# Optimization experiments

Measured on AMD Instinct MI355X. Metric: run time of the kernel, lower is better.

The kernel has to match this reference:

```python
import jax, jax.numpy as jnp
import numpy as np

HEAD = 8
C = 32  # dhead
SCALE = 0.17677669529663687  # 1/sqrt(32)


def setup_inputs() -> dict:
    key = jax.random.key(0)
    k1, k2, k3, k4 = jax.random.split(key, 4)
    N, S, R, M = 1, 256, 384, 256
    msa_repr = jax.random.normal(k1, (N, S, R, M), dtype=jnp.float32)
    # 0.02 init scale keeps softmax logits / sigmoid pre-activations in a sane range
    gate_proj = jax.random.normal(k2, (M, M), dtype=jnp.float32) * 0.02
    qkv_proj = jax.random.normal(k3, (M, 3 * M), dtype=jnp.float32) * 0.02
    out_proj = jax.random.normal(k4, (M, M), dtype=jnp.float32) * 0.02
    return {"msa_repr": msa_repr, "gate_proj": gate_proj, "qkv_proj": qkv_proj, "out_proj": out_proj}


def reference(msa_repr, gate_proj, qkv_proj, out_proj):
    # col_attn: permute [N,S,R,M] -> [N,R,S,M]; attention runs over the residue axis S
    x = jnp.transpose(msa_repr, (0, 2, 1, 3))  # [N,R,S,M]
    N, R, S, M = x.shape
    gate = jax.nn.sigmoid(x @ gate_proj).reshape(N, R, S, HEAD, C)
    q, k, v = jnp.split(x @ qkv_proj, 3, axis=-1)  # each [N,R,S,M]
    q = q.reshape(N, R, S, HEAD, C)
    k = k.reshape(N, R, S, HEAD, C)
    v = v.reshape(N, R, S, HEAD, C)
    sim = jnp.einsum('nrihc,nrjhc->nrhij', q, k) * jnp.float32(SCALE)  # [N,R,H,S,S]
    attn = jax.nn.softmax(sim, axis=-1)
    out = jnp.einsum('nrhij,nrjhc->nrihc', attn, v) * gate  # [N,R,S,H,C]
    out = out.reshape(N, R, S, HEAD * C) @ out_proj  # [N,R,S,M]
    return jnp.transpose(out, (0, 2, 1, 3))  # back to [N,S,R,M]
```

## Files before the change

### kernel.cpp

```cpp
#include <hip/hip_runtime.h>
#include <hip/hip_bf16.h>

#define R_DIM 384
#define S_DIM 256
#define M_DIM 256

typedef __attribute__((ext_vector_type(4))) float  f32x4;
typedef __attribute__((ext_vector_type(4))) float  fvec4;
typedef __attribute__((ext_vector_type(8))) short  short8;
typedef __attribute__((ext_vector_type(4))) short  short4v;

__device__ __forceinline__ short f2bf(float f) {
    __hip_bfloat16 h = __float2bfloat16(f);
    return __builtin_bit_cast(short, h);
}
__device__ __forceinline__ float bf2f(short s) {
    return __bfloat162float(__builtin_bit_cast(__hip_bfloat16, s));
}

__device__ __forceinline__ void gload_lds16(const void* gsrc, void* ldst) {
    __builtin_amdgcn_global_load_lds(
        (const __attribute__((address_space(1))) unsigned int*)gsrc,
        (__attribute__((address_space(3))) unsigned int*)ldst, 16, 0, 0);
}

#define QSCALE (0.17677669529663687f * 1.4426950408889634f)

__global__ __launch_bounds__(256) void k_prep(
    const float* __restrict__ gp, const float* __restrict__ qkvp,
    const float* __restrict__ op, short* __restrict__ Wt1,
    short* __restrict__ Wot)
{
    __shared__ float tile[64][65];
    const int tx = threadIdx.x & 63, ty = threadIdx.x >> 6;
    const int k0 = blockIdx.x * 64;
    const int j0 = blockIdx.y * 64;
    const float* src; int ld, cb;
    if (j0 < 256)       { src = gp;   ld = 256; cb = j0; }
    else if (j0 < 1024) { src = qkvp; ld = 768; cb = j0 - 256; }
    else                { src = op;   ld = 256; cb = j0 - 1024; }
    for (int q = 0; q < 16; ++q) {
        const int kk = q * 4 + ty;
        tile[kk][tx] = src[(k0 + kk) * ld + cb + tx];
    }
    __syncthreads();
    for (int q = 0; q < 16; ++q) {
        const int jj = q * 4 + ty;
        const int jglob = j0 + jj;
        const float scl = (jglob >= 256 && jglob < 512) ? QSCALE : 1.0f;
        const float val = tile[tx][jj] * scl;
        if (jglob < 1024) Wt1[jglob * 256 + k0 + tx] = f2bf(val);
        else              Wot[(jglob - 1024) * 256 + k0 + tx] = f2bf(val);
    }
}

__global__ __launch_bounds__(256, 3) void k_qkvgate(
    const float* __restrict__ msa, const short* __restrict__ Wt1,
    short* __restrict__ gate, short* __restrict__ qb,
    short* __restrict__ kb, short* __restrict__ vb)
{
    __shared__ __align__(16) char Al[64 * 512];
    __shared__ __align__(16) short Bl[2][128 * 32];
    const int tid = threadIdx.x;
    const int l = tid & 63, w = tid >> 6;
    const int wr = w >> 1, wc = w & 1;
    const int rowBase = blockIdx.x * 64;

    {
        const int arow0 = tid >> 6;
        const int col4  = (tid & 63) * 4;
        const int slot  = (tid & 63) >> 1;
        const int sub   = (tid & 63) & 1;
        for (int ii = 0; ii < 16; ++ii) {
            const int a_r = ii * 4 + arow0;
            const int i = rowBase + a_r;
            const int rr = i >> 8, ss = i & 255;
            fvec4 vv = *(const fvec4*)(msa + ((ss * R_DIM + rr) << 8) + col4);
            short4v b4;
            b4.x = f2bf(vv.x); b4.y = f2bf(vv.y);
            b4.z = f2bf(vv.z); b4.w = f2bf(vv.w);
            *(short4v*)(Al + a_r * 512 + ((slot ^ (a_r & 7)) << 4) + sub * 8) = b4;
        }
    }

    auto stageB = [&](int tt, short* buf) {
        const int cb = (tt >> 3) * 128, k0 = (tt & 7) * 32;
        #pragma unroll
        for (int r = 0; r < 2; ++r) {
            const int L = r * 256 + w * 64 + l;
            const int row = L >> 2, psl = L & 3;
            const int gsl = psl ^ ((row >> 1) & 3);
            gload_lds16(Wt1 + (cb + row) * 256 + k0 + gsl * 8,
                        buf + (r * 256 + w * 64) * 8);
        }
    };

    stageB(0, (short*)Bl[0]);
    __syncthreads();

    short8 af[8][2];
    #pragma unroll
    for (int kc = 0; kc < 8; ++kc) {
        const int aslot = kc * 4 + (l >> 4);
        #pragma unroll
        for (int it = 0; it < 2; ++it) {
            const int row = wr * 32 + it * 16 + (l & 15);
            af[kc][it] = *(const short8*)(Al + row * 512 + ((aslot ^ (row & 7)) << 4));
        }
    }

    short* AlT = (short*)Al;
    const int rr_blk = rowBase >> 8;
    const int ssBase = rowBase & 255;

    f32x4 acc[2][4] = {};
    for (int ct = 0; ct < 8; ++ct) {
        #pragma unroll
        for (int kc = 0; kc < 8; ++kc) {
            const int t = ct * 8 + kc;
            if (t + 1 < 64) stageB(t + 1, (short*)Bl[(kc + 1) & 1]);

            const short* Bb = (const short*)Bl[kc & 1];
            short8 bfr[4];
            #pragma unroll
            for (int jt = 0; jt < 4; ++jt) {
                const int row = wc * 64 + jt * 16 + (l & 15);
                const int psl = (l >> 4) ^ ((row >> 1) & 3);
                bfr[jt] = *(const short8*)(Bb + row * 32 + psl * 8);
            }
            #pragma unroll
            for (int it = 0; it < 2; ++it)
                #pragma unroll
                for (int jt = 0; jt < 4; ++jt)
                    acc[it][jt] = __builtin_amdgcn_mfma_f32_16x16x32_bf16(
                        af[kc][it], bfr[jt], acc[it][jt], 0, 0, 0);

            __syncthreads();
        }
        const int colBase = ct * 128;
        const int sel = ct >> 1;
        if (sel < 3) {
            short* dst = (sel == 0) ? gate : (sel == 1) ? qb : kb;
            #pragma unroll
            for (int it = 0; it < 2; ++it) {
                const int base_i = rowBase + wr * 32 + it * 16 + ((l >> 4) << 2);
                #pragma unroll
                for (int reg = 0; reg < 4; ++reg) {
                    const int i = base_i + reg;
                    const int rr = i >> 8, ss = i & 255;
                    #pragma unroll
                    for (int jt = 0; jt < 4; ++jt) {
                        const int jg = colBase + wc * 64 + jt * 16 + (l & 15);
                        const int jj = jg & 255;
                        const int h = jj >> 5, c = jj & 31;
                        float vv = acc[it][jt][reg];
                        if (sel == 0) vv = 1.0f / (1.0f + __builtin_amdgcn_exp2f(-vv * 1.4426950408889634f));
                        dst[(((rr << 3) + h) * 256 + ss) * 32 + c] = f2bf(vv);
                    }
                }
            }
        } else {
            const int jjBase = (colBase & 255);
            #pragma unroll
            for (int it = 0; it < 2; ++it) {
                const int ssL0 = wr * 32 + it * 16 + ((l >> 4) << 2);
                #pragma unroll
                for (int reg = 0; reg < 4; ++reg) {
                    #pragma unroll
                    for (int jt = 0; jt < 4; ++jt) {
                        const int jjL = wc * 64 + jt * 16 + (l & 15);
                        AlT[jjL * 72 + ssL0 + reg] = f2bf(acc[it][jt][reg]);
                    }
                }
            }
            __syncthreads();
            #pragma unroll
            for (int q = 0; q < 4; ++q) {
                const int cid = q * 256 + tid;
                const int jjL = cid >> 3, sc = cid & 7;
                short8 vv8 = *(const short8*)(&AlT[jjL * 72 + sc * 8]);
                const int jj = jjBase + jjL;
                const int h = jj >> 5, c = jj & 31;
                const int pp = (rr_blk << 3) + h;
                *(short8*)(vb + (pp << 13) + (c << 8) + ssBase + sc * 8) = vv8;
            }
        }
        #pragma unroll
        for (int it = 0; it < 2; ++it)
            #pragma unroll
            for (int jt = 0; jt < 4; ++jt)
                acc[it][jt] = (f32x4){0.f, 0.f, 0.f, 0.f};
    }
}

__global__ __launch_bounds__(256) void k_attn(
    short* qo, const short* __restrict__ kb, const short* __restrict__ vb,
    const short* __restrict__ gate)
{
    __shared__ __align__(16) short Pl[4 * 32 * 68];
    const int tid = threadIdx.x;
    const int l = tid & 63, w = tid >> 6;
    const int p = blockIdx.x;
    short* qg = qo + p * 8192;
    const short* kg = kb + p * 8192;
    const short* vg = vb + p * 8192;
    const short* gg = gate + p * 8192;
    const int c0 = (l >> 4) * 8;

    short8 qf[4];
    #pragma unroll
    for (int it = 0; it < 4; ++it) {
        const int s = w * 64 + it * 16 + (l & 15);
        qf[it] = *(const short8*)(qg + s * 32 + c0);
    }

    f32x4 oacc[4][2] = {};
    f32x4 ssum[4] = {};
    short8 bones;
    #pragma unroll
    for (int e = 0; e < 8; ++e) bones[e] = (short)0x3F80;
    short* Pw = &Pl[w * (32 * 68)];

    for (int ch = 0; ch < 4; ++ch) {
        const int j0 = ch * 64;
        f32x4 sacc[4][4] = {};
        short8 kf[4];
        #pragma unroll
        for (int jt = 0; jt < 4; ++jt) {
            const int row = j0 + jt * 16 + (l & 15);
            kf[jt] = *(const short8*)(kg + row * 32 + c0);
        }
        #pragma unroll
        for (int it = 0; it < 4; ++it)
            #pragma unroll
            for (int jt = 0; jt < 4; ++jt)
                sacc[it][jt] = __builtin_amdgcn_mfma_f32_16x16x32_bf16(
                    qf[it], kf[jt], sacc[it][jt], 0, 0, 0);

        short8 vfa[2][2];
        #pragma unroll
        for (int kk = 0; kk < 2; ++kk)
            #pragma unroll
            for (int cti = 0; cti < 2; ++cti)
                vfa[kk][cti] = *(const short8*)(
                    vg + (cti * 16 + (l & 15)) * 256 + j0 + kk * 32 + (l >> 4) * 8);

        #pragma unroll
        for (int ih = 0; ih < 2; ++ih) {
            #pragma unroll
            for (int itl = 0; itl < 2; ++itl) {
                const int it = ih * 2 + itl;
                #pragma unroll
                for (int reg = 0; reg < 4; ++reg) {
                    const int rowl = itl * 16 + ((l >> 4) << 2) + reg;
                    #pragma unroll
                    for (int jt = 0; jt < 4; ++jt)
                        Pw[rowl * 68 + jt * 16 + (l & 15)] =
                            f2bf(__builtin_amdgcn_exp2f(sacc[it][jt][reg]));
                }
            }
            #pragma unroll
            for (int kk = 0; kk < 2; ++kk) {
                const int koff = kk * 32 + (l >> 4) * 8;
                short8 pf[2];
                #pragma unroll
                for (int itl = 0; itl < 2; ++itl)
                    pf[itl] = *(const short8*)(&Pw[(itl * 16 + (l & 15)) * 68 + koff]);
                #pragma unroll
                for (int itl = 0; itl < 2; ++itl) {
                    const int it = ih * 2 + itl;
                    #pragma unroll
                    for (int cti = 0; cti < 2; ++cti)
                        oacc[it][cti] = __builtin_amdgcn_mfma_f32_16x16x32_bf16(
                            pf[itl], vfa[kk][cti], oacc[it][cti], 0, 0, 0);
                    ssum[it] = __builtin_amdgcn_mfma_f32_16x16x32_bf16(
                        pf[itl], bones, ssum[it], 0, 0, 0);
                }
            }
        }
    }
    #pragma unroll
    for (int it = 0; it < 4; ++it) {
        #pragma unroll
        for (int reg = 0; reg < 4; ++reg) {
            const float inv = 1.0f / ssum[it][reg];
            const int s = w * 64 + it * 16 + ((l >> 4) << 2) + reg;
            #pragma unroll
            for (int cti = 0; cti < 2; ++cti) {
                const int c = cti * 16 + (l & 15);
                const float gv = bf2f(gg[s * 32 + c]);
                qg[s * 32 + c] = f2bf(oacc[it][cti][reg] * inv * gv);
            }
        }
    }
}

__global__ __launch_bounds__(256) void k_out(
    const short* __restrict__ ao, const short* __restrict__ Wot,
    float* __restrict__ out)
{
    __shared__ __align__(16) char Al[128 * 128];
    __shared__ __align__(16) char Bl[128 * 128];
    const int tid = threadIdx.x;
    const int l = tid & 63, w = tid >> 6;
    const int wr = w >> 1, wc = w & 1;
    const int rowBase = blockIdx.y * 128;
    const int colBase = blockIdx.x * 128;
    f32x4 acc[4][4] = {};
    for (int kidx = 0; kidx < 4; ++kidx) {
        const int k0 = kidx * 64;
        {
            const int slot = tid & 7;
            const int rb = tid >> 3;
            const int kin = k0 + slot * 8;
            const int h = kin >> 5, c0 = kin & 31;
            #pragma unroll
            for (int ii = 0; ii < 4; ++ii) {
                const int a_r = ii * 32 + rb;
                const int i = rowBase + a_r;
                const int rr = i >> 8, ss = i & 255;
                short8 av = *(const short8*)(ao + (((rr << 3) + h) * 256 + ss) * 32 + c0);
                *(short8*)(Al + a_r * 128 + ((slot ^ (a_r & 7)) << 4)) = av;
            }
            #pragma unroll
            for (int jj = 0; jj < 4; ++jj) {
                const int j_r = jj * 32 + rb;
                short8 wv = *(const short8*)(Wot + (colBase + j_r) * 256 + k0 + slot * 8);
                *(short8*)(Bl + j_r * 128 + ((slot ^ (j_r & 7)) << 4)) = wv;
            }
        }
        __syncthreads();
        #pragma unroll
        for (int kh = 0; kh < 2; ++kh) {
            short8 af[4], bfr[4];
            const int sl = kh * 4 + (l >> 4);
            #pragma unroll
            for (int it = 0; it < 4; ++it) {
                const int row = wr * 64 + it * 16 + (l & 15);
                af[it] = *(const short8*)(Al + row * 128 + ((sl ^ (row & 7)) << 4));
            }
            #pragma unroll
            for (int jt = 0; jt < 4; ++jt) {
                const int row = wc * 64 + jt * 16 + (l & 15);
                bfr[jt] = *(const short8*)(Bl + row * 128 + ((sl ^ (row & 7)) << 4));
            }
            #pragma unroll
            for (int it = 0; it < 4; ++it)
                #pragma unroll
                for (int jt = 0; jt < 4; ++jt)
                    acc[it][jt] = __builtin_amdgcn_mfma_f32_16x16x32_bf16(
                        af[it], bfr[jt], acc[it][jt], 0, 0, 0);
        }
        __syncthreads();
    }
    #pragma unroll
    for (int it = 0; it < 4; ++it) {
        const int base_i = rowBase + wr * 64 + it * 16 + ((l >> 4) << 2);
        #pragma unroll
        for (int reg = 0; reg < 4; ++reg) {
            const int i = base_i + reg;
            const int rr = i >> 8, ss = i & 255;
            #pragma unroll
            for (int jt = 0; jt < 4; ++jt) {
                const int m = colBase + wc * 64 + jt * 16 + (l & 15);
                out[((ss * R_DIM + rr) << 8) + m] = acc[it][jt][reg];
            }
        }
    }
}

extern "C" void kernel_launch(void* const* d_in, const int* in_sizes, int n_in,
                              void* d_out, int out_size, void* d_ws, size_t ws_size,
                              hipStream_t stream) {
    const float* msa  = (const float*)d_in[0];
    const float* gp   = (const float*)d_in[1];
    const float* qkvp = (const float*)d_in[2];
    const float* op   = (const float*)d_in[3];
    float* out = (float*)d_out;
    char* ws = (char*)d_ws;

    const size_t SZ = 50331648;
    short* Wt1  = (short*)ws;
    short* Wot  = (short*)(ws + 524288);
    short* gate = (short*)(ws + 655360);
    short* qb   = (short*)(ws + 655360 + 1 * SZ);
    short* kb   = (short*)(ws + 655360 + 2 * SZ);
    short* vb   = (short*)(ws + 655360 + 3 * SZ);

    k_prep<<<dim3(4, 20), 256, 0, stream>>>(gp, qkvp, op, Wt1, Wot);
    k_qkvgate<<<dim3(1536), 256, 0, stream>>>(msa, Wt1, gate, qb, kb, vb);
    k_attn<<<dim3(3072), 256, 0, stream>>>(qb, kb, vb, gate);
    k_out<<<dim3(2, 768), 256, 0, stream>>>(qb, Wot, out);
}
```

Baseline: 225.1 us.

## Double-buffer out-proj weights via direct global-to-LDS loads, read activations from registers

Reworks the output-projection GEMM: the weight tile is staged with async global_load_lds into a double-buffered LDS region, prefetching the next k-chunk while computing the current one. Activation fragments are loaded straight from global memory into registers instead of going through LDS. It also adds an occupancy hint of 4 blocks per CU and shrinks the LDS footprint. This aims to overlap weight loads with MFMA work and cut LDS traffic and syncs, at the cost of uncoalesced-ish direct global A reads and more k-iterations with barriers.

```diff
diff --git a/kernel.cpp b/kernel.cpp
--- a/kernel.cpp
+++ b/kernel.cpp
@@ -295,62 +295,59 @@
     }
 }
 
-__global__ __launch_bounds__(256) void k_out(
+__global__ __launch_bounds__(256, 4) void k_out(
     const short* __restrict__ ao, const short* __restrict__ Wot,
     float* __restrict__ out)
 {
-    __shared__ __align__(16) char Al[128 * 128];
-    __shared__ __align__(16) char Bl[128 * 128];
+    __shared__ __align__(16) short Bl[2][128 * 32];
     const int tid = threadIdx.x;
     const int l = tid & 63, w = tid >> 6;
     const int wr = w >> 1, wc = w & 1;
     const int rowBase = blockIdx.y * 128;
     const int colBase = blockIdx.x * 128;
+
+    auto stageB = [&](int kc, short* buf) {
+        const int k0 = kc * 32;
+        #pragma unroll
+        for (int r = 0; r < 2; ++r) {
+            const int L = r * 256 + w * 64 + l;
+            const int row = L >> 2, psl = L & 3;
+            const int gsl = psl ^ ((row >> 1) & 3);
+            gload_lds16(Wot + (colBase + row) * 256 + k0 + gsl * 8,
+                        buf + (r * 256 + w * 64) * 8);
+        }
+    };
+
+    stageB(0, (short*)Bl[0]);
+    __syncthreads();
+
     f32x4 acc[4][4] = {};
-    for (int kidx = 0; kidx < 4; ++kidx) {
-        const int k0 = kidx * 64;
-        {
-            const int slot = tid & 7;
-            const int rb = tid >> 3;
-            const int kin = k0 + slot * 8;
-            const int h = kin >> 5, c0 = kin & 31;
-            #pragma unroll
-            for (int ii = 0; ii < 4; ++ii) {
-                const int a_r = ii * 32 + rb;
-                const int i = rowBase + a_r;
-                const int rr = i >> 8, ss = i & 255;
-                short8 av = *(const short8*)(ao + (((rr << 3) + h) * 256 + ss) * 32 + c0);
-                *(short8*)(Al + a_r * 128 + ((slot ^ (a_r & 7)) << 4)) = av;
-            }
-            #pragma unroll
-            for (int jj = 0; jj < 4; ++jj) {
-                const int j_r = jj * 32 + rb;
-                short8 wv = *(const short8*)(Wot + (colBase + j_r) * 256 + k0 + slot * 8);
-                *(short8*)(Bl + j_r * 128 + ((slot ^ (j_r & 7)) << 4)) = wv;
-            }
-        }
-        __syncthreads();
-        #pragma unroll
-        for (int kh = 0; kh < 2; ++kh) {
-            short8 af[4], bfr[4];
-            const int sl = kh * 4 + (l >> 4);
-            #pragma unroll
-            for (int it = 0; it < 4; ++it) {
-                const int row = wr * 64 + it * 16 + (l & 15);
-                af[it] = *(const short8*)(Al + row * 128 + ((sl ^ (row & 7)) << 4));
-            }
-            #pragma unroll
-            for (int jt = 0; jt < 4; ++jt) {
-                const int row = wc * 64 + jt * 16 + (l & 15);
-                bfr[jt] = *(const short8*)(Bl + row * 128 + ((sl ^ (row & 7)) << 4));
-            }
-            #pragma unroll
-            for (int it = 0; it < 4; ++it)
-                #pragma unroll
-                for (int jt = 0; jt < 4; ++jt)
-                    acc[it][jt] = __builtin_amdgcn_mfma_f32_16x16x32_bf16(
-                        af[it], bfr[jt], acc[it][jt], 0, 0, 0);
-        }
+    #pragma unroll
+    for (int kc = 0; kc < 8; ++kc) {
+        if (kc + 1 < 8) stageB(kc + 1, (short*)Bl[(kc + 1) & 1]);
+
+        short8 af[4];
+        #pragma unroll
+        for (int it = 0; it < 4; ++it) {
+            const int i = rowBase + wr * 64 + it * 16 + (l & 15);
+            const int rr = i >> 8, ss = i & 255;
+            af[it] = *(const short8*)(ao + (((rr << 3) + kc) * 256 + ss) * 32 + (l >> 4) * 8);
+        }
+        const short* Bb = (const short*)Bl[kc & 1];
+        short8 bfr[4];
+        #pragma unroll
+        for (int jt = 0; jt < 4; ++jt) {
+            const int row = wc * 64 + jt * 16 + (l & 15);
+            const int psl = (l >> 4) ^ ((row >> 1) & 3);
+            bfr[jt] = *(const short8*)(Bb + row * 32 + psl * 8);
+        }
+        #pragma unroll
+        for (int it = 0; it < 4; ++it)
+            #pragma unroll
+            for (int jt = 0; jt < 4; ++jt)
+                acc[it][jt] = __builtin_amdgcn_mfma_f32_16x16x32_bf16(
+                    af[it], bfr[jt], acc[it][jt], 0, 0, 0);
+
         __syncthreads();
     }
     #pragma unroll
```

Result: no change. 222.0 us (-1.4%).
